# Kernel tuning notes

Hardware: AMD Instinct MI355X
Metric: run time of the kernel (lower is better)

## Reference

```python
import jax, jax.numpy as jnp
import numpy as np

B, C, L = 32, 8, 2048
K, S = 512, 64  # num_shapelets, shapelets_size


def setup_inputs() -> dict:
    key = jax.random.key(0)
    k1, k2 = jax.random.split(key)
    x = jax.random.normal(k1, (B, C, L), dtype=jnp.float32)
    shapelets = jax.random.normal(k2, (C, K, S), dtype=jnp.float32)
    return {"x": x, "shapelets": shapelets}


def reference(x, shapelets):
    # x: [B, C, L]; shapelets: [C, K, S]
    s = shapelets.shape[-1]
    n_dims = x.shape[1]
    W = x.shape[2] - s + 1  # number of sliding windows
    # unfold(2, S, 1): gather overlapping windows -> [B, C, W, S]
    idx = jnp.arange(W)[:, None] + jnp.arange(s)[None, :]
    xw = x[:, :, idx]
    # L2-normalize windows along window length (clamp min like torch)
    xw = xw / jnp.maximum(jnp.linalg.norm(xw, axis=-1, keepdims=True), 1e-8)
    # L2-normalize shapelets along length
    sn = shapelets / jnp.maximum(jnp.linalg.norm(shapelets, axis=-1, keepdims=True), 1e-8)
    # matmul [B,C,W,S] @ [C,S,K] then sum over C, fused into one einsum -> [B, W, K]
    sim = jnp.einsum('bcws,cks->bwk', xw, sn) / n_dims
    sim = jax.nn.relu(sim)
    # max over window positions -> [B, K]; keep the singleton channel dim like torch ([B,1,K])
    out = jnp.max(sim, axis=1)
    return out[:, None, :]
```

## Files before the change

### kernel.cpp

```cpp
#include <hip/hip_runtime.h>


#define B_ 32
#define C_ 8
#define L_ 2048
#define K_ 512
#define S_ 64
#define W_ 1985
#define TW 128

typedef _Float16 f16x8 __attribute__((ext_vector_type(8)));
typedef _Float16 f16x8u __attribute__((ext_vector_type(8), aligned(4)));
typedef float f32x16 __attribute__((ext_vector_type(16)));

__global__ __launch_bounds__(256)
void prep_k(const float* __restrict__ x, const float* __restrict__ sh,
            _Float16* __restrict__ Bp, _Float16* __restrict__ xh0,
            _Float16* __restrict__ xh1, _Float16* __restrict__ invh,
            float* __restrict__ out) {
    __shared__ float xr[L_];
    const int tid = threadIdx.x;
    const int blk = blockIdx.x;

    if (blk < 128) {
        const int sb   = blk * 4 + (tid >> 6);
        const int c    = sb >> 6;
        const int kq   = (sb >> 4) & 3;
        const int nt   = sb & 15;
        const int lane = tid & 63;
        const int half = lane >> 5;
        const int q    = nt * 32 + (lane & 31);

        const float4* sp = (const float4*)(sh + (size_t)(c * K_ + q) * S_);
        float ss = 0.f;
        #pragma unroll
        for (int i = 0; i < 8; ++i) {
            float4 v = sp[half * 8 + i];
            ss += v.x * v.x + v.y * v.y + v.z * v.z + v.w * v.w;
        }
        ss += __shfl_xor(ss, 32);
        float inv = 1.f / fmaxf(sqrtf(ss), 1e-8f);

        float4 u0 = sp[kq * 4 + half * 2];
        float4 u1 = sp[kq * 4 + half * 2 + 1];
        f16x8 o;
        o[0] = (_Float16)(u0.x * inv); o[1] = (_Float16)(u0.y * inv);
        o[2] = (_Float16)(u0.z * inv); o[3] = (_Float16)(u0.w * inv);
        o[4] = (_Float16)(u1.x * inv); o[5] = (_Float16)(u1.y * inv);
        o[6] = (_Float16)(u1.z * inv); o[7] = (_Float16)(u1.w * inv);
        ((f16x8*)Bp)[((c * 4 + kq) * 16 + nt) * 64 + lane] = o;
    } else {
        const int r = blk - 128;
        const float* xp = x + (size_t)r * L_;
        for (int i = tid; i < L_ / 4; i += 256)
            ((float4*)xr)[i] = ((const float4*)xp)[i];
        __syncthreads();

        {
            const int i = tid * 8;
            f16x8 a, bsh;
            #pragma unroll
            for (int j = 0; j < 8; ++j) {
                a[j]   = (_Float16)xr[i + j];
                int n  = i + j + 1;
                bsh[j] = (_Float16)(n < L_ ? xr[n] : 0.f);
            }
            *(f16x8*)(xh0 + (size_t)r * L_ + i) = a;
            *(f16x8*)(xh1 + (size_t)r * L_ + i) = bsh;
        }

        _Float16* ivp = invh + (size_t)r * L_;
        const int w0 = tid * 8;
        float ss = 0.f;
        if (w0 < W_) {
            #pragma unroll
            for (int j = 0; j < S_; ++j) { float v = xr[w0 + j]; ss += v * v; }
        }
        #pragma unroll
        for (int u = 0; u < 8; ++u) {
            int w = w0 + u;
            float o = 0.f;
            if (u > 0 && w < W_)
                ss += xr[w + 63] * xr[w + 63] - xr[w - 1] * xr[w - 1];
            if (w < W_) o = 0.125f / fmaxf(sqrtf(ss), 1e-8f);
            if (w < L_) ivp[w] = (_Float16)o;
        }
        if (r < 64) out[r * 256 + tid] = 0.f;
    }
}

__global__ __launch_bounds__(256, 4)
void mcs_k(const _Float16* __restrict__ Bp, const _Float16* __restrict__ xh0,
           const _Float16* __restrict__ xh1, const _Float16* __restrict__ invh,
           float* __restrict__ out) {
    const int wt  = blockIdx.x;
    const int ng  = blockIdx.y;
    const int b   = blockIdx.z;
    const int tid = threadIdx.x;
    const int lane = tid & 63;
    const int wv   = tid >> 6;
    const int mg   = wv >> 1;
    const int nw   = wv & 1;

    const int l31 = lane & 31;
    const int lh  = lane >> 5;
    const int Wb  = wt * TW + mg * 64;
    const int par = l31 & 1;

    const _Float16* xb  = (par ? xh1 - 1 : xh0) + (size_t)(b * C_) * L_;
    const _Float16* ivb = invh + (size_t)(b * C_) * L_;
    const f16x8* Bq     = (const f16x8*)Bp;
    const int coloff    = (ng * 4 + nw * 2) * 64 + lane;

    f16x8  Bbuf[3][2];
    f16x8u Abuf[2][2];
    _Float16 ivr[2][2];

    auto issueB = [&](int s, int slot) {
        const int c = s >> 2, ks = s & 3;
        const f16x8* bb = Bq + ((c * 4 + ks) * 16) * 64 + coloff;
        Bbuf[slot][0] = bb[0];
        Bbuf[slot][1] = bb[64];
    };
    auto issueA = [&](int s, int slot) {
        const int c = s >> 2, ks = s & 3;
        const _Float16* xr = xb + c * L_;
        #pragma unroll
        for (int mt = 0; mt < 2; ++mt) {
            int p  = Wb + mt * 32 + l31 + ks * 16 + lh * 8;
            int pc = p <= L_ - 8 ? p : L_ - 8;
            Abuf[slot][mt] = *(const f16x8u*)(xr + pc);
        }
    };

    ivr[0][0] = ivb[Wb + l31];
    ivr[0][1] = ivb[Wb + 32 + l31];
    issueB(0, 0);
    issueA(0, 0);
    issueB(1, 1);

    f32x16 acc[2][2];
    #pragma unroll
    for (int mt = 0; mt < 2; ++mt)
        #pragma unroll
        for (int nt = 0; nt < 2; ++nt)
            #pragma unroll
            for (int r = 0; r < 16; ++r) acc[mt][nt][r] = 0.f;

    #pragma unroll
    for (int s = 0; s < 32; ++s) {
        const int c = s >> 2, ks = s & 3;
        if (s + 2 < 32) issueB(s + 2, (s + 2) % 3);
        if (s + 1 < 32) issueA(s + 1, (s + 1) & 1);
        if (ks == 0 && c + 1 < C_) {
            const _Float16* ivn = ivb + (c + 1) * L_;
            ivr[(c + 1) & 1][0] = ivn[Wb + l31];
            ivr[(c + 1) & 1][1] = ivn[Wb + 32 + l31];
        }
        f16x8 af0 = (f16x8)Abuf[s & 1][0] * ivr[c & 1][0];
        f16x8 af1 = (f16x8)Abuf[s & 1][1] * ivr[c & 1][1];

        #pragma unroll
        for (int nt = 0; nt < 2; ++nt) {
            acc[0][nt] = __builtin_amdgcn_mfma_f32_32x32x16_f16(
                af0, Bbuf[s % 3][nt], acc[0][nt], 0, 0, 0);
            acc[1][nt] = __builtin_amdgcn_mfma_f32_32x32x16_f16(
                af1, Bbuf[s % 3][nt], acc[1][nt], 0, 0, 0);
        }
    }

    #pragma unroll
    for (int nt = 0; nt < 2; ++nt) {
        float m = 0.f;
        #pragma unroll
        for (int mt = 0; mt < 2; ++mt)
            #pragma unroll
            for (int r = 0; r < 16; ++r)
                m = fmaxf(m, acc[mt][nt][r]);
        m = fmaxf(m, __shfl_xor(m, 32));
        if (lane < 32)
            atomicMax((unsigned int*)(out + b * K_ + ng * 128 + nw * 64 + nt * 32 + l31),
                      __float_as_uint(m));
    }
}

extern "C" void kernel_launch(void* const* d_in, const int* in_sizes, int n_in,
                              void* d_out, int out_size, void* d_ws, size_t ws_size,
                              hipStream_t stream) {
    const float* x  = (const float*)d_in[0];
    const float* sh = (const float*)d_in[1];
    float* out = (float*)d_out;

    char* ws = (char*)d_ws;
    _Float16* Bp   = (_Float16*)ws;
    _Float16* xh0  = (_Float16*)(ws + (512 << 10));
    _Float16* xh1  = (_Float16*)(ws + (512 << 10) + (1 << 20));
    _Float16* invh = (_Float16*)(ws + (512 << 10) + (2 << 20));

    prep_k<<<dim3(384), dim3(256), 0, stream>>>(x, sh, Bp, xh0, xh1, invh, out);
    mcs_k<<<dim3(16, 4, B_), dim3(256), 0, stream>>>(Bp, xh0, xh1, invh, out);
}
```

Before: 115.8 us.

## Keep shapelet B fragments in registers and loop over window tiles per block

The main kernel now loads each wave's full 32-step B fragment set into registers once. Each block then loops over eight 64-window tiles, using a 3-deep A prefetch ring and double-buffered inverse norms, and keeps a running max across tiles. The x and inverse-norm buffers are padded to 2176 elements with zeroed tails, which removes the clamping on A loads. The grid shrinks from 2048 to 512 blocks and launch bounds drop to 2 blocks per CU, trading occupancy and parallelism for less B reloading and fewer atomics.

New measurement: 136.5 us. +17.9%, slower.

```diff
diff --git a/kernel.cpp b/kernel.cpp
--- a/kernel.cpp
+++ b/kernel.cpp
@@ -7,7 +7,7 @@
 #define K_ 512
 #define S_ 64
 #define W_ 1985
-#define TW 128
+#define LP 2176
 
 typedef _Float16 f16x8 __attribute__((ext_vector_type(8)));
 typedef _Float16 f16x8u __attribute__((ext_vector_type(8), aligned(4)));
@@ -65,11 +65,19 @@
                 int n  = i + j + 1;
                 bsh[j] = (_Float16)(n < L_ ? xr[n] : 0.f);
             }
-            *(f16x8*)(xh0 + (size_t)r * L_ + i) = a;
-            *(f16x8*)(xh1 + (size_t)r * L_ + i) = bsh;
-        }
-
-        _Float16* ivp = invh + (size_t)r * L_;
+            *(f16x8*)(xh0 + (size_t)r * LP + i) = a;
+            *(f16x8*)(xh1 + (size_t)r * LP + i) = bsh;
+        }
+        if (tid < 16) {
+            f16x8 z;
+            #pragma unroll
+            for (int j = 0; j < 8; ++j) z[j] = (_Float16)0.f;
+            *(f16x8*)(xh0  + (size_t)r * LP + L_ + tid * 8) = z;
+            *(f16x8*)(xh1  + (size_t)r * LP + L_ + tid * 8) = z;
+            *(f16x8*)(invh + (size_t)r * LP + L_ + tid * 8) = z;
+        }
+
+        _Float16* ivp = invh + (size_t)r * LP;
         const int w0 = tid * 8;
         float ss = 0.f;
         if (w0 < W_) {
@@ -89,99 +97,88 @@
     }
 }
 
-__global__ __launch_bounds__(256, 4)
+struct IvT { _Float16 v[8][2]; };
+
+__global__ __launch_bounds__(256, 2)
 void mcs_k(const _Float16* __restrict__ Bp, const _Float16* __restrict__ xh0,
            const _Float16* __restrict__ xh1, const _Float16* __restrict__ invh,
            float* __restrict__ out) {
-    const int wt  = blockIdx.x;
-    const int ng  = blockIdx.y;
+    const int mh  = blockIdx.x;
+    const int kg  = blockIdx.y;
     const int b   = blockIdx.z;
     const int tid = threadIdx.x;
     const int lane = tid & 63;
     const int wv   = tid >> 6;
-    const int mg   = wv >> 1;
-    const int nw   = wv & 1;
-
-    const int l31 = lane & 31;
-    const int lh  = lane >> 5;
-    const int Wb  = wt * TW + mg * 64;
-    const int par = l31 & 1;
-
-    const _Float16* xb  = (par ? xh1 - 1 : xh0) + (size_t)(b * C_) * L_;
-    const _Float16* ivb = invh + (size_t)(b * C_) * L_;
-    const f16x8* Bq     = (const f16x8*)Bp;
-    const int coloff    = (ng * 4 + nw * 2) * 64 + lane;
-
-    f16x8  Bbuf[3][2];
-    f16x8u Abuf[2][2];
-    _Float16 ivr[2][2];
-
-    auto issueB = [&](int s, int slot) {
-        const int c = s >> 2, ks = s & 3;
-        const f16x8* bb = Bq + ((c * 4 + ks) * 16) * 64 + coloff;
-        Bbuf[slot][0] = bb[0];
-        Bbuf[slot][1] = bb[64];
+    const int colg = kg * 4 + wv;
+    const int l31  = lane & 31;
+    const int lh   = lane >> 5;
+    const int par  = l31 & 1;
+    const int W0   = mh * 512;
+
+    const _Float16* xb  = (par ? xh1 - 1 : xh0) + (size_t)(b * C_) * LP;
+    const _Float16* ivb = invh + (size_t)(b * C_) * LP;
+
+    f16x8 Breg[32];
+    {
+        const f16x8* Bq = (const f16x8*)Bp + colg * 64 + lane;
+        #pragma unroll
+        for (int s = 0; s < 32; ++s) Breg[s] = Bq[s * 16 * 64];
+    }
+
+    f16x8u Ar[8];
+    auto issueA = [&](int t, int s, int mt, int slot) {
+        int c = s >> 2, ks = s & 3;
+        int p = W0 + t * 64 + mt * 32 + l31 + ks * 16 + lh * 8;
+        Ar[slot] = *(const f16x8u*)(xb + c * LP + p);
     };
-    auto issueA = [&](int s, int slot) {
-        const int c = s >> 2, ks = s & 3;
-        const _Float16* xr = xb + c * L_;
-        #pragma unroll
-        for (int mt = 0; mt < 2; ++mt) {
-            int p  = Wb + mt * 32 + l31 + ks * 16 + lh * 8;
-            int pc = p <= L_ - 8 ? p : L_ - 8;
-            Abuf[slot][mt] = *(const f16x8u*)(xr + pc);
-        }
+    auto loadIv = [&](int t) -> IvT {
+        IvT r;
+        int tc = t < 8 ? t : 0;
+        #pragma unroll
+        for (int c = 0; c < 8; ++c) {
+            r.v[c][0] = ivb[c * LP + W0 + tc * 64 + l31];
+            r.v[c][1] = ivb[c * LP + W0 + tc * 64 + 32 + l31];
+        }
+        return r;
     };
 
-    ivr[0][0] = ivb[Wb + l31];
-    ivr[0][1] = ivb[Wb + 32 + l31];
-    issueB(0, 0);
-    issueA(0, 0);
-    issueB(1, 1);
-
-    f32x16 acc[2][2];
     #pragma unroll
-    for (int mt = 0; mt < 2; ++mt)
-        #pragma unroll
-        for (int nt = 0; nt < 2; ++nt)
-            #pragma unroll
-            for (int r = 0; r < 16; ++r) acc[mt][nt][r] = 0.f;
-
-    #pragma unroll
-    for (int s = 0; s < 32; ++s) {
-        const int c = s >> 2, ks = s & 3;
-        if (s + 2 < 32) issueB(s + 2, (s + 2) % 3);
-        if (s + 1 < 32) issueA(s + 1, (s + 1) & 1);
-        if (ks == 0 && c + 1 < C_) {
-            const _Float16* ivn = ivb + (c + 1) * L_;
-            ivr[(c + 1) & 1][0] = ivn[Wb + l31];
-            ivr[(c + 1) & 1][1] = ivn[Wb + 32 + l31];
-        }
-        f16x8 af0 = (f16x8)Abuf[s & 1][0] * ivr[c & 1][0];
-        f16x8 af1 = (f16x8)Abuf[s & 1][1] * ivr[c & 1][1];
-
-        #pragma unroll
-        for (int nt = 0; nt < 2; ++nt) {
-            acc[0][nt] = __builtin_amdgcn_mfma_f32_32x32x16_f16(
-                af0, Bbuf[s % 3][nt], acc[0][nt], 0, 0, 0);
-            acc[1][nt] = __builtin_amdgcn_mfma_f32_32x32x16_f16(
-                af1, Bbuf[s % 3][nt], acc[1][nt], 0, 0, 0);
+    for (int s = 0; s < 3; ++s) { issueA(0, s, 0, (s * 2) & 7); issueA(0, s, 1, (s * 2 + 1) & 7); }
+    IvT ivA = loadIv(0), ivB;
+
+    float mx = 0.f;
+    f32x16 acc0, acc1;
+
+    #pragma unroll 1
+    for (int tp = 0; tp < 4; ++tp) {
+        #pragma unroll
+        for (int hf = 0; hf < 2; ++hf) {
+            const int t = tp * 2 + hf;
+            #pragma unroll
+            for (int r = 0; r < 16; ++r) { acc0[r] = 0.f; acc1[r] = 0.f; }
+            #pragma unroll
+            for (int s = 0; s < 32; ++s) {
+                int ps = s + 3;
+                int pt = t + (ps >> 5), pss = ps & 31;
+                issueA(pt, pss, 0, (ps * 2) & 7);
+                issueA(pt, pss, 1, (ps * 2 + 1) & 7);
+                if (s == 8) { if (hf) ivA = loadIv(t + 1); else ivB = loadIv(t + 1); }
+                const IvT& iv = hf ? ivB : ivA;
+                int c = s >> 2;
+                f16x8 af0 = (f16x8)Ar[(s * 2) & 7] * iv.v[c][0];
+                f16x8 af1 = (f16x8)Ar[(s * 2 + 1) & 7] * iv.v[c][1];
+                acc0 = __builtin_amdgcn_mfma_f32_32x32x16_f16(af0, Breg[s], acc0, 0, 0, 0);
+                acc1 = __builtin_amdgcn_mfma_f32_32x32x16_f16(af1, Breg[s], acc1, 0, 0, 0);
+            }
+            #pragma unroll
+            for (int r = 0; r < 16; ++r) mx = fmaxf(mx, fmaxf(acc0[r], acc1[r]));
         }
     }
 
-    #pragma unroll
-    for (int nt = 0; nt < 2; ++nt) {
-        float m = 0.f;
-        #pragma unroll
-        for (int mt = 0; mt < 2; ++mt)
-            #pragma unroll
-            for (int r = 0; r < 16; ++r)
-                m = fmaxf(m, acc[mt][nt][r]);
-        m = fmaxf(m, __shfl_xor(m, 32));
-        if (lane < 32)
-            atomicMax((unsigned int*)(out + b * K_ + ng * 128 + nw * 64 + nt * 32 + l31),
-                      __float_as_uint(m));
-    }
+    mx = fmaxf(mx, __shfl_xor(mx, 32));
+    if (lane < 32)
+        atomicMax((unsigned int*)(out + b * K_ + colg * 32 + l31),
+                  __float_as_uint(mx));
 }
 
 extern "C" void kernel_launch(void* const* d_in, const int* in_sizes, int n_in,
@@ -192,11 +189,12 @@
     float* out = (float*)d_out;
 
     char* ws = (char*)d_ws;
+    const size_t xhN = (size_t)B_ * C_ * LP * sizeof(_Float16);
     _Float16* Bp   = (_Float16*)ws;
     _Float16* xh0  = (_Float16*)(ws + (512 << 10));
-    _Float16* xh1  = (_Float16*)(ws + (512 << 10) + (1 << 20));
-    _Float16* invh = (_Float16*)(ws + (512 << 10) + (2 << 20));
+    _Float16* xh1  = (_Float16*)(ws + (512 << 10) + xhN);
+    _Float16* invh = (_Float16*)(ws + (512 << 10) + 2 * xhN);
 
     prep_k<<<dim3(384), dim3(256), 0, stream>>>(x, sh, Bp, xh0, xh1, invh, out);
-    mcs_k<<<dim3(16, 4, B_), dim3(256), 0, stream>>>(Bp, xh0, xh1, invh, out);
+    mcs_k<<<dim3(4, 4, B_), dim3(256), 0, stream>>>(Bp, xh0, xh1, invh, out);
 }
```
